# Optimization experiments

Measured on AMD Instinct MI355X. Metric: run time of the kernel, lower is better.

The kernel has to match this reference:

```python
import jax, jax.numpy as jnp
import numpy as np

B, F, S, H = 8, 512, 8192, 8
D = F // H
GROUPS = F // 16  # GroupNorm group_cnt = channels // 16
EPS = 1e-8


def group_norm(x, gamma, beta):
    # x: [B, C, S]; normalize per (group-channels, spatial) like torch GroupNorm
    b, c, s = x.shape
    xg = x.reshape(b, GROUPS, c // GROUPS, s)
    mu = xg.mean(axis=(2, 3), keepdims=True)
    var = xg.var(axis=(2, 3), keepdims=True)
    xn = ((xg - mu) * jax.lax.rsqrt(var + EPS)).reshape(b, c, s)
    return xn * gamma[None, :, None] + beta[None, :, None]


def setup_inputs() -> dict:
    key = jax.random.key(0)
    ks = jax.random.split(key, 5)
    return {
        "hidden_states": jax.random.normal(ks[0], (B, F, S), jnp.float32),
        "qkv_w": jax.random.normal(ks[1], (3, H, D, F), jnp.float32) * 0.02,
        "qkv_b": jnp.zeros((3, 1, 1, H, D), jnp.float32),
        "out_proj": jax.random.normal(ks[2], (F, F), jnp.float32) * 0.02,
        "gn1_gamma": jnp.ones((F,), jnp.float32),
        "gn1_beta": jnp.zeros((F,), jnp.float32),
        "gn2_gamma": jnp.ones((F,), jnp.float32),
        "gn2_beta": jnp.zeros((F,), jnp.float32),
        # torch init is zeros; use small random so the gated branch is exercised
        "gate_g": jax.random.normal(ks[3], (F, 1), jnp.float32) * 0.1,
    }


def reference(hidden_states, qkv_w, qkv_b, out_proj,
              gn1_gamma, gn1_beta, gn2_gamma, gn2_beta, gate_g):
    x = group_norm(hidden_states, gn1_gamma, gn1_beta)
    # [3, B, S, H, D]
    qkv = jnp.einsum('bfl,ihdf->iblhd', x, qkv_w) + qkv_b
    q = jax.nn.elu(qkv[0]) + 1.0
    k = jax.nn.elu(qkv[1]) + 1.0
    v = qkv[2]
    # global non-causal linear attention: KV = sum_l k_l v_l^T  -> [B,H,D,D]
    kv = jnp.einsum('blhf,blhF->bhFf', k, v)
    k_sum = jnp.sum(k, axis=1, keepdims=True)               # [B,1,H,D]
    z = jnp.sum(q * k_sum, axis=-1, keepdims=True)          # [B,S,H,1]
    qz = q / z
    out = jnp.einsum('blhf,bhFf->blhF', qz, kv)             # [B,S,H,D]
    out = out.reshape(out.shape[0], out.shape[1], -1)       # [B,S,F]
    y = jnp.einsum('blf,Ff->bFl', out, out_proj)            # [B,F,S]
    y = group_norm(y, gn2_gamma, gn2_beta)
    # rezero-style gate: residual + per-channel gate * branch
    return hidden_states + gate_g[None] * y
```

## Files before the change

### kernel.cpp

```cpp
#include <hip/hip_runtime.h>
#include <hip/hip_bf16.h>

#define BB 8
#define FF 512
#define SS 8192
#define HH 8
#define DD 64
#define N1 1536

typedef __hip_bfloat16 bf16;
typedef __attribute__((ext_vector_type(8))) short bf16x8;
typedef __attribute__((ext_vector_type(4))) float f32x4;

__device__ __forceinline__ float us2f(unsigned short u) {
    union { unsigned int i; float f; } x; x.i = ((unsigned int)u) << 16; return x.f;
}
__device__ __forceinline__ unsigned short f2b(float f) {
    unsigned int u = __builtin_bit_cast(unsigned int, f);
    return (unsigned short)((u + 0x7FFFu + ((u >> 16) & 1u)) >> 16);
}
__device__ __forceinline__ void gll16(const void* g, void* l) {
    __builtin_amdgcn_global_load_lds((const __attribute__((address_space(1))) void*)g,
                                     (__attribute__((address_space(3))) void*)l, 16, 0, 0);
}
__device__ __forceinline__ bf16x8 fragld(const unsigned short* base, int row, int quad) {
    int off = row * 32 + (((quad + (row >> 1)) & 3) << 3);
    return *(const bf16x8*)(base + off);
}

__global__ void gn1_part(const float* __restrict__ hid, float* __restrict__ part) {
    int bg = blockIdx.x;
    const float4* base = (const float4*)(hid + ((size_t)(bg >> 5) * FF + (bg & 31) * 16) * SS);
    float s = 0.f, s2 = 0.f;
    int t0 = blockIdx.y * 4096 + threadIdx.x;
    #pragma unroll
    for (int it = 0; it < 16; it++) {
        float4 x = base[t0 + it * 256];
        s  += x.x + x.y + x.z + x.w;
        s2 += x.x * x.x + x.y * x.y + x.z * x.z + x.w * x.w;
    }
    #pragma unroll
    for (int off = 32; off > 0; off >>= 1) {
        s  += __shfl_down(s, off, 64);
        s2 += __shfl_down(s2, off, 64);
    }
    __shared__ float rs_[8];
    int wid = threadIdx.x >> 6, lane = threadIdx.x & 63;
    if (lane == 0) { rs_[wid] = s; rs_[wid + 4] = s2; }
    __syncthreads();
    if (threadIdx.x == 0)
        atomicAdd(&part[bg * 2], rs_[0] + rs_[1] + rs_[2] + rs_[3]);
    else if (threadIdx.x == 64)
        atomicAdd(&part[bg * 2 + 1], rs_[4] + rs_[5] + rs_[6] + rs_[7]);
}

__global__ void gn2_part(const unsigned short* __restrict__ y, float* __restrict__ part) {
    int bg = blockIdx.x;
    const bf16x8* base = (const bf16x8*)(y + ((size_t)(bg >> 5) * FF + (bg & 31) * 16) * SS);
    float s = 0.f, s2 = 0.f;
    int t0 = blockIdx.y * 2048 + threadIdx.x;
    #pragma unroll
    for (int it = 0; it < 8; it++) {
        bf16x8 u = base[t0 + it * 256];
        #pragma unroll
        for (int k = 0; k < 8; k++) {
            float a = us2f((unsigned short)u[k]);
            s += a; s2 += a * a;
        }
    }
    #pragma unroll
    for (int off = 32; off > 0; off >>= 1) {
        s  += __shfl_down(s, off, 64);
        s2 += __shfl_down(s2, off, 64);
    }
    __shared__ float rs_[8];
    int wid = threadIdx.x >> 6, lane = threadIdx.x & 63;
    if (lane == 0) { rs_[wid] = s; rs_[wid + 4] = s2; }
    __syncthreads();
    if (threadIdx.x == 0)
        atomicAdd(&part[bg * 2], rs_[0] + rs_[1] + rs_[2] + rs_[3]);
    else if (threadIdx.x == 64)
        atomicAdd(&part[bg * 2 + 1], rs_[4] + rs_[5] + rs_[6] + rs_[7]);
}

__global__ void gn_final(const float* __restrict__ part, const float* __restrict__ gamma,
                         const float* __restrict__ beta, const float* __restrict__ gate,
                         float* __restrict__ sc, float* __restrict__ sh) {
    int c = blockIdx.x * 256 + threadIdx.x;
    int ch = c & 511;
    int bg = (c >> 9) * 32 + (ch >> 4);
    float ts = part[bg * 2], ts2 = part[bg * 2 + 1];
    float mu  = ts * (1.f / 131072.f);
    float var = ts2 * (1.f / 131072.f) - mu * mu;
    float r   = rsqrtf(var + 1e-8f);
    float scv = gamma[ch] * r;
    float shv = beta[ch] - mu * scv;
    if (gate) { float gv = gate[ch]; scv *= gv; shv *= gv; }
    sc[c] = scv; sh[c] = shv;
}

__global__ void castb(const float* __restrict__ s, unsigned short* __restrict__ d, int n4) {
    int i = blockIdx.x * 256 + threadIdx.x;
    if (i >= n4) return;
    float4 v = ((const float4*)s)[i];
    ushort4 u = make_ushort4(f2b(v.x), f2b(v.y), f2b(v.z), f2b(v.w));
    ((ushort4*)d)[i] = u;
}

__global__ void xn_prep(const float* __restrict__ hid, const float* __restrict__ sc,
                        const float* __restrict__ sh, unsigned short* __restrict__ xnA) {
    int b = blockIdx.z, f0 = blockIdx.y * 64, l0 = blockIdx.x * 64;
    __shared__ float t[64][65];
    int tid = threadIdx.x;
    #pragma unroll
    for (int it = 0; it < 16; it++) {
        int idx = it * 256 + tid;
        int f = idx >> 6, l = idx & 63;
        int fg = f0 + f;
        t[f][l] = hid[((size_t)b * FF + fg) * SS + l0 + l] * sc[b * FF + fg] + sh[b * FF + fg];
    }
    __syncthreads();
    #pragma unroll
    for (int it = 0; it < 4; it++) {
        int idx = it * 256 + tid;
        int l = idx >> 4, fq = (idx & 15) * 4;
        ushort4 u = make_ushort4(f2b(t[fq + 0][l]), f2b(t[fq + 1][l]),
                                 f2b(t[fq + 2][l]), f2b(t[fq + 3][l]));
        *(ushort4*)(xnA + ((size_t)b * SS + l0 + l) * FF + f0 + fq) = u;
    }
}

__global__ __launch_bounds__(256) void gemm1_mfma(
    const unsigned short* __restrict__ A, const unsigned short* __restrict__ Bw,
    const float* __restrict__ bias,
    unsigned short* __restrict__ q, unsigned short* __restrict__ kT,
    unsigned short* __restrict__ vT) {
    __shared__ unsigned short smem[16384] __attribute__((aligned(16)));
    unsigned short* As = smem;
    unsigned short* Bs = smem + 4096;
    const int b = blockIdx.z;
    const int m0 = blockIdx.x * 128, n0 = blockIdx.y * 128;
    const int tid = threadIdx.x;
    const int w = tid >> 6, ln = tid & 63;
    const int wr = w >> 1, wc = w & 1;
    const int lrow = ln & 15, quad = ln >> 4;

    const int ch0 = tid, ch1 = tid + 256;
    const int r0 = ch0 >> 2, c0 = ((ch0 & 3) - (r0 >> 1)) & 3;
    const int r1 = ch1 >> 2, c1 = ((ch1 & 3) - (r1 >> 1)) & 3;
    const unsigned short* pA0 = A + ((size_t)b * SS + m0 + r0) * FF + c0 * 8;
    const unsigned short* pA1 = A + ((size_t)b * SS + m0 + r1) * FF + c1 * 8;
    const unsigned short* pB0 = Bw + (size_t)(n0 + r0) * FF + c0 * 8;
    const unsigned short* pB1 = Bw + (size_t)(n0 + r1) * FF + c1 * 8;
    unsigned short* lA0 = As + ch0 * 8; unsigned short* lA1 = As + ch1 * 8;
    unsigned short* lB0 = Bs + ch0 * 8; unsigned short* lB1 = Bs + ch1 * 8;

    f32x4 acc[4][4];
    #pragma unroll
    for (int j = 0; j < 4; j++)
        #pragma unroll
        for (int i = 0; i < 4; i++) acc[j][i] = (f32x4){0.f, 0.f, 0.f, 0.f};

    for (int kk = 0; kk < 16; kk++) {
        gll16(pA0, lA0); gll16(pA1, lA1); gll16(pB0, lB0); gll16(pB1, lB1);
        pA0 += 32; pA1 += 32; pB0 += 32; pB1 += 32;
        __syncthreads();
        bf16x8 af[4], bm[4];
        #pragma unroll
        for (int j = 0; j < 4; j++) af[j] = fragld(Bs, wc * 64 + j * 16 + lrow, quad);
        #pragma unroll
        for (int i = 0; i < 4; i++) bm[i] = fragld(As, wr * 64 + i * 16 + lrow, quad);
        #pragma unroll
        for (int j = 0; j < 4; j++)
            #pragma unroll
            for (int i = 0; i < 4; i++)
                acc[j][i] = __builtin_amdgcn_mfma_f32_16x16x32_bf16(af[j], bm[i], acc[j][i], 0, 0, 0);
        __syncthreads();
    }
    const int n0v = n0 + wc * 64;
    const int sel = n0 >> 9;
    if (sel == 0) {
        const int nchb = (wc << 3) + (quad >> 1);
        const int nin  = (quad & 1) << 2;
        #pragma unroll
        for (int j = 0; j < 4; j++) {
            const float* bp = bias + n0v + j * 16 + (quad << 2);
            float b0 = bp[0], b1 = bp[1], b2 = bp[2], b3 = bp[3];
            #pragma unroll
            for (int i = 0; i < 4; i++) {
                float v0 = acc[j][i][0] + b0, v1 = acc[j][i][1] + b1;
                float v2 = acc[j][i][2] + b2, v3 = acc[j][i][3] + b3;
                v0 = v0 > 0.f ? v0 + 1.f : __expf(v0);
                v1 = v1 > 0.f ? v1 + 1.f : __expf(v1);
                v2 = v2 > 0.f ? v2 + 1.f : __expf(v2);
                v3 = v3 > 0.f ? v3 + 1.f : __expf(v3);
                int m = (wr << 6) + (i << 4) + lrow;
                int chk = (nchb + (j << 1)) ^ (m & 7);
                *(ushort4*)(smem + m * 128 + (chk << 3) + nin) =
                    make_ushort4(f2b(v0), f2b(v1), f2b(v2), f2b(v3));
            }
        }
        __syncthreads();
        const size_t rowb = (size_t)b * SS + m0;
        const int cc = tid & 15, rr = tid >> 4;
        #pragma unroll
        for (int p = 0; p < 8; p++) {
            int m = (p << 4) + rr;
            bf16x8 v = *(const bf16x8*)(smem + m * 128 + ((cc ^ (m & 7)) << 3));
            *(bf16x8*)(q + (rowb + m) * FF + n0 + (cc << 3)) = v;
        }
    } else {
        unsigned short* outp = (sel == 1) ? kT : vT;
        const int nbase = n0 & 511;
        #pragma unroll
        for (int j = 0; j < 4; j++) {
            const float* bp = bias + n0v + j * 16 + (quad << 2);
            float bb[4] = {bp[0], bp[1], bp[2], bp[3]};
            #pragma unroll
            for (int i = 0; i < 4; i++) {
                int m = (wr << 6) + (i << 4) + lrow;
                int mch = m >> 3, mi = m & 7;
                #pragma unroll
                for (int r = 0; r < 4; r++) {
                    float val = acc[j][i][r] + bb[r];
                    if (sel == 1) val = val > 0.f ? val + 1.f : __expf(val);
                    int n = (wc << 6) + (j << 4) + (quad << 2) + r;
                    smem[n * 128 + ((mch ^ ((n >> 2) & 7)) << 3) + mi] = f2b(val);
                }
            }
        }
        __syncthreads();
        const int cc = tid & 15, rr = tid >> 4;
        #pragma unroll
        for (int p = 0; p < 8; p++) {
            int n = (p << 4) + rr;
            bf16x8 v = *(const bf16x8*)(smem + n * 128 + ((cc ^ ((n >> 2) & 7)) << 3));
            int nrel = nbase + n;
            *(bf16x8*)(outp + (((size_t)b * HH + (nrel >> 6)) * DD + (nrel & 63)) * SS
                       + m0 + (cc << 3)) = v;
        }
    }
}

__global__ __launch_bounds__(256) void kv_mfma(
    const unsigned short* __restrict__ kT, const unsigned short* __restrict__ vT,
    float* __restrict__ kv, float* __restrict__ ksum) {
    const int bh = blockIdx.x;
    const int l0 = blockIdx.y * 512;
    const int tid = threadIdx.x;

    {
        int f = tid >> 2, part = tid & 3;
        const unsigned short* kp = kT + ((size_t)bh * DD + f) * SS + l0 + part * 128;
        float s = 0.f;
        #pragma unroll
        for (int c = 0; c < 16; c++) {
            bf16x8 u = *(const bf16x8*)(kp + c * 8);
            #pragma unroll
            for (int j = 0; j < 8; j++) s += us2f((unsigned short)u[j]);
        }
        s += __shfl_down(s, 1, 64);
        s += __shfl_down(s, 2, 64);
        if (part == 0) atomicAdd(&ksum[bh * DD + f], s);
    }

    const int w = tid >> 6, ln = tid & 63;
    const int lrow = ln & 15, quad = ln >> 4;
    f32x4 acc[4];
    #pragma unroll
    for (int ft = 0; ft < 4; ft++) acc[ft] = (f32x4){0.f, 0.f, 0.f, 0.f};
    const unsigned short* vbase = vT + ((size_t)bh * DD + w * 16 + lrow) * SS + l0;
    const unsigned short* kbase = kT + ((size_t)bh * DD + lrow) * SS + l0;
    for (int ks = 0; ks < 16; ks++) {
        bf16x8 vf = *(const bf16x8*)(vbase + ks * 32 + quad * 8);
        #pragma unroll
        for (int ft = 0; ft < 4; ft++) {
            bf16x8 kf = *(const bf16x8*)(kbase + (size_t)(ft * 16) * SS + ks * 32 + quad * 8);
            acc[ft] = __builtin_amdgcn_mfma_f32_16x16x32_bf16(vf, kf, acc[ft], 0, 0, 0);
        }
    }
    float* kvp = kv + (size_t)bh * 4096;
    #pragma unroll
    for (int ft = 0; ft < 4; ft++) {
        #pragma unroll
        for (int r = 0; r < 4; r++) {
            int e = w * 16 + (quad << 2) + r;
            int f = ft * 16 + lrow;
            atomicAdd(&kvp[e * 64 + f], acc[ft][r]);
        }
    }
}

__global__ void kvcast(const float* __restrict__ kv, unsigned short* __restrict__ kv16) {
    int i = blockIdx.x * 256 + threadIdx.x;
    float4 v = ((const float4*)kv)[i];
    ((ushort4*)kv16)[i] = make_ushort4(f2b(v.x), f2b(v.y), f2b(v.z), f2b(v.w));
}

__global__ __launch_bounds__(256) void attn_mfma(
    const unsigned short* __restrict__ q, const unsigned short* __restrict__ kv16,
    const float* __restrict__ ksum, unsigned short* __restrict__ attn) {
    const int bh = blockIdx.y, b = bh >> 3, h = bh & 7;
    const int l0 = blockIdx.x * 128;
    __shared__ float ksS[64];
    __shared__ float zS[128];
    const int tid = threadIdx.x;
    if (tid < 64) ksS[tid] = ksum[bh * DD + tid];
    __syncthreads();
    if (tid < 128) {
        const unsigned short* qp = q + ((size_t)b * SS + l0 + tid) * FF + h * DD;
        float z = 0.f;
        #pragma unroll
        for (int c = 0; c < 8; c++) {
            bf16x8 u = *(const bf16x8*)(qp + c * 8);
            #pragma unroll
            for (int j = 0; j < 8; j++) z += us2f((unsigned short)u[j]) * ksS[c * 8 + j];
        }
        zS[tid] = 1.f / z;
    }
    __syncthreads();

    const int w = tid >> 6, ln = tid & 63;
    const int lrow = ln & 15, quad = ln >> 4;
    const unsigned short* kvp = kv16 + (size_t)bh * 4096;
    bf16x8 kvf[4][2];
    #pragma unroll
    for (int et = 0; et < 4; et++)
        #pragma unroll
        for (int ks = 0; ks < 2; ks++)
            kvf[et][ks] = *(const bf16x8*)(kvp + (et * 16 + lrow) * 64 + ks * 32 + quad * 8);

    f32x4 acc[2][4];
    #pragma unroll
    for (int lt = 0; lt < 2; lt++)
        #pragma unroll
        for (int et = 0; et < 4; et++) acc[lt][et] = (f32x4){0.f, 0.f, 0.f, 0.f};

    const unsigned short* qbase = q + ((size_t)b * SS + l0 + w * 32) * FF + h * DD;
    #pragma unroll
    for (int lt = 0; lt < 2; lt++) {
        #pragma unroll
        for (int ks = 0; ks < 2; ks++) {
            bf16x8 qf = *(const bf16x8*)(qbase + (size_t)(lt * 16 + lrow) * FF + ks * 32 + quad * 8);
            #pragma unroll
            for (int et = 0; et < 4; et++)
                acc[lt][et] = __builtin_amdgcn_mfma_f32_16x16x32_bf16(kvf[et][ks], qf, acc[lt][et], 0, 0, 0);
        }
    }
    #pragma unroll
    for (int lt = 0; lt < 2; lt++) {
        int lloc = w * 32 + lt * 16 + lrow;
        float zi = zS[lloc];
        unsigned short* op = attn + ((size_t)b * SS + l0 + lloc) * FF + h * DD;
        #pragma unroll
        for (int et = 0; et < 4; et++) {
            ushort4 u = make_ushort4(f2b(acc[lt][et][0] * zi), f2b(acc[lt][et][1] * zi),
                                     f2b(acc[lt][et][2] * zi), f2b(acc[lt][et][3] * zi));
            *(ushort4*)(op + et * 16 + (quad << 2)) = u;
        }
    }
}

__global__ __launch_bounds__(256) void gemm2_mfma(
    const unsigned short* __restrict__ A, const unsigned short* __restrict__ Bw,
    unsigned short* __restrict__ y) {
    __shared__ unsigned short smem[16384] __attribute__((aligned(16)));
    unsigned short* As = smem;
    unsigned short* Bs = smem + 4096;
    const int b = blockIdx.z;
    const int m0 = blockIdx.x * 128, n0 = blockIdx.y * 128;
    const int tid = threadIdx.x;
    const int w = tid >> 6, ln = tid & 63;
    const int wr = w >> 1, wc = w & 1;
    const int lrow = ln & 15, quad = ln >> 4;

    const int ch0 = tid, ch1 = tid + 256;
    const int r0 = ch0 >> 2, c0 = ((ch0 & 3) - (r0 >> 1)) & 3;
    const int r1 = ch1 >> 2, c1 = ((ch1 & 3) - (r1 >> 1)) & 3;
    const unsigned short* pA0 = A + ((size_t)b * SS + m0 + r0) * FF + c0 * 8;
    const unsigned short* pA1 = A + ((size_t)b * SS + m0 + r1) * FF + c1 * 8;
    const unsigned short* pB0 = Bw + (size_t)(n0 + r0) * FF + c0 * 8;
    const unsigned short* pB1 = Bw + (size_t)(n0 + r1) * FF + c1 * 8;
    unsigned short* lA0 = As + ch0 * 8; unsigned short* lA1 = As + ch1 * 8;
    unsigned short* lB0 = Bs + ch0 * 8; unsigned short* lB1 = Bs + ch1 * 8;

    f32x4 acc[4][4];
    #pragma unroll
    for (int i = 0; i < 4; i++)
        #pragma unroll
        for (int j = 0; j < 4; j++) acc[i][j] = (f32x4){0.f, 0.f, 0.f, 0.f};

    for (int kk = 0; kk < 16; kk++) {
        gll16(pA0, lA0); gll16(pA1, lA1); gll16(pB0, lB0); gll16(pB1, lB1);
        pA0 += 32; pA1 += 32; pB0 += 32; pB1 += 32;
        __syncthreads();
        bf16x8 am[4], bn[4];
        #pragma unroll
        for (int i = 0; i < 4; i++) am[i] = fragld(As, wr * 64 + i * 16 + lrow, quad);
        #pragma unroll
        for (int j = 0; j < 4; j++) bn[j] = fragld(Bs, wc * 64 + j * 16 + lrow, quad);
        #pragma unroll
        for (int i = 0; i < 4; i++)
            #pragma unroll
            for (int j = 0; j < 4; j++)
                acc[i][j] = __builtin_amdgcn_mfma_f32_16x16x32_bf16(am[i], bn[j], acc[i][j], 0, 0, 0);
        __syncthreads();
    }
    #pragma unroll
    for (int i = 0; i < 4; i++) {
        const int mch = (wr << 3) + (i << 1) + (quad >> 1);
        const int min_ = (quad & 1) << 2;
        #pragma unroll
        for (int j = 0; j < 4; j++) {
            int n = (wc << 6) + (j << 4) + lrow;
            int chk = mch ^ (n & 7);
            *(ushort4*)(smem + n * 128 + (chk << 3) + min_) =
                make_ushort4(f2b(acc[i][j][0]), f2b(acc[i][j][1]),
                             f2b(acc[i][j][2]), f2b(acc[i][j][3]));
        }
    }
    __syncthreads();
    const int cc = tid & 15, rr = tid >> 4;
    #pragma unroll
    for (int p = 0; p < 8; p++) {
        int n = (p << 4) + rr;
        bf16x8 v = *(const bf16x8*)(smem + n * 128 + ((cc ^ (n & 7)) << 3));
        *(bf16x8*)(y + ((size_t)b * FF + n0 + n) * SS + m0 + (cc << 3)) = v;
    }
}

__global__ void final_kernel(const float* __restrict__ hid, const bf16* __restrict__ y,
                             const float* __restrict__ gsc, const float* __restrict__ gsh,
                             float* __restrict__ out) {
    int bf = blockIdx.x;
    float a = gsc[bf], c0 = gsh[bf];
    const float4*  hp = (const float4*)(hid + (size_t)bf * SS);
    const ushort4* yp = (const ushort4*)(y + (size_t)bf * SS);
    float4* op = (float4*)(out + (size_t)bf * SS);
    for (int t = threadIdx.x; t < 2048; t += 256) {
        float4 hv = hp[t];
        ushort4 yv = yp[t];
        float4 r;
        r.x = hv.x + a * us2f(yv.x) + c0;
        r.y = hv.y + a * us2f(yv.y) + c0;
        r.z = hv.z + a * us2f(yv.z) + c0;
        r.w = hv.w + a * us2f(yv.w) + c0;
        op[t] = r;
    }
}

extern "C" void kernel_launch(void* const* d_in, const int* in_sizes, int n_in,
                              void* d_out, int out_size, void* d_ws, size_t ws_size,
                              hipStream_t stream) {
    const float* hid      = (const float*)d_in[0];
    const float* qkv_w    = (const float*)d_in[1];
    const float* qkv_b    = (const float*)d_in[2];
    const float* out_proj = (const float*)d_in[3];
    const float* g1       = (const float*)d_in[4];
    const float* b1       = (const float*)d_in[5];
    const float* g2       = (const float*)d_in[6];
    const float* b2       = (const float*)d_in[7];
    const float* gate     = (const float*)d_in[8];
    float* out = (float*)d_out;

    char* p = (char*)d_ws;
    float* sc1 = (float*)p; p += (size_t)4096 * 4;
    float* sh1 = (float*)p; p += (size_t)4096 * 4;
    float* gsc = (float*)p; p += (size_t)4096 * 4;
    float* gsh = (float*)p; p += (size_t)4096 * 4;
    float* kvb = (float*)p; p += (size_t)262144 * 4;
    float* ksm = (float*)p; p += (size_t)4096 * 4;
    float* gnp = (float*)p; p += (size_t)1024 * 4;
    unsigned short* kv16 = (unsigned short*)p; p += (size_t)262144 * 2;
    unsigned short* Wb = (unsigned short*)p; p += (size_t)786432 * 2;
    unsigned short* Pb = (unsigned short*)p; p += (size_t)262144 * 2;
    unsigned short* qb = (unsigned short*)p; p += (size_t)33554432 * 2;
    unsigned short* kTb = (unsigned short*)p; p += (size_t)33554432 * 2;
    unsigned short* vTb = (unsigned short*)p;
    unsigned short* attn = kTb;
    unsigned short* yb   = vTb;
    unsigned short* xnA  = (unsigned short*)d_out;

    hipMemsetAsync(kvb, 0, (size_t)(262144 + 4096 + 1024) * 4, stream);

    gn1_part<<<dim3(256, 8), 256, 0, stream>>>(hid, gnp);
    gn_final<<<16, 256, 0, stream>>>(gnp, g1, b1, nullptr, sc1, sh1);
    castb<<<768, 256, 0, stream>>>(qkv_w, Wb, 196608);
    castb<<<256, 256, 0, stream>>>(out_proj, Pb, 65536);
    xn_prep<<<dim3(128, 8, 8), 256, 0, stream>>>(hid, sc1, sh1, xnA);
    gemm1_mfma<<<dim3(64, 12, 8), 256, 0, stream>>>(xnA, Wb, qkv_b, qb, kTb, vTb);
    kv_mfma<<<dim3(64, 16), 256, 0, stream>>>(kTb, vTb, kvb, ksm);
    kvcast<<<256, 256, 0, stream>>>(kvb, kv16);
    attn_mfma<<<dim3(64, 64), 256, 0, stream>>>(qb, kv16, ksm, attn);
    gemm2_mfma<<<dim3(64, 4, 8), 256, 0, stream>>>(attn, Pb, yb);
    gn2_part<<<dim3(256, 8), 256, 0, stream>>>((const unsigned short*)yb, gnp + 512);
    gn_final<<<16, 256, 0, stream>>>(gnp + 512, g2, b2, gate, gsc, gsh);
    final_kernel<<<4096, 256, 0, stream>>>(hid, (const bf16*)yb, gsc, gsh, out);
}
```

Before: 651.6 us.

## Fuse GroupNorm2 stats into gemm2 epilogue, widen K tiles, split gemm1 by output

The GroupNorm2 partial-sum reduction now runs in the gemm2 epilogue, using shuffle reductions and atomics, so the separate gn2_part pass over y is removed. Both GEMMs now load 64-wide K tiles with an XOR swizzle, which halves the number of loop iterations and barriers. gemm1 is split into two template instantiations. The K/V instance swaps the MFMA operand order so its accumulators can be written straight to the transposed kT/vT layout. Both GEMM epilogues drop the LDS staging and write ushort4 directly to global memory, which may give less coalesced stores. The fused epilogue also adds more atomics.

```diff
diff --git a/kernel.cpp b/kernel.cpp
--- a/kernel.cpp
+++ b/kernel.cpp
@@ -23,9 +23,8 @@
     __builtin_amdgcn_global_load_lds((const __attribute__((address_space(1))) void*)g,
                                      (__attribute__((address_space(3))) void*)l, 16, 0, 0);
 }
-__device__ __forceinline__ bf16x8 fragld(const unsigned short* base, int row, int quad) {
-    int off = row * 32 + (((quad + (row >> 1)) & 3) << 3);
-    return *(const bf16x8*)(base + off);
+__device__ __forceinline__ bf16x8 fragld64(const unsigned short* base, int row, int kq) {
+    return *(const bf16x8*)(base + row * 64 + ((kq ^ (row & 7)) << 3));
 }
 
 __global__ void gn1_part(const float* __restrict__ hid, float* __restrict__ part) {
@@ -38,35 +37,6 @@
         float4 x = base[t0 + it * 256];
         s  += x.x + x.y + x.z + x.w;
         s2 += x.x * x.x + x.y * x.y + x.z * x.z + x.w * x.w;
-    }
-    #pragma unroll
-    for (int off = 32; off > 0; off >>= 1) {
-        s  += __shfl_down(s, off, 64);
-        s2 += __shfl_down(s2, off, 64);
-    }
-    __shared__ float rs_[8];
-    int wid = threadIdx.x >> 6, lane = threadIdx.x & 63;
-    if (lane == 0) { rs_[wid] = s; rs_[wid + 4] = s2; }
-    __syncthreads();
-    if (threadIdx.x == 0)
-        atomicAdd(&part[bg * 2], rs_[0] + rs_[1] + rs_[2] + rs_[3]);
-    else if (threadIdx.x == 64)
-        atomicAdd(&part[bg * 2 + 1], rs_[4] + rs_[5] + rs_[6] + rs_[7]);
-}
-
-__global__ void gn2_part(const unsigned short* __restrict__ y, float* __restrict__ part) {
-    int bg = blockIdx.x;
-    const bf16x8* base = (const bf16x8*)(y + ((size_t)(bg >> 5) * FF + (bg & 31) * 16) * SS);
-    float s = 0.f, s2 = 0.f;
-    int t0 = blockIdx.y * 2048 + threadIdx.x;
-    #pragma unroll
-    for (int it = 0; it < 8; it++) {
-        bf16x8 u = base[t0 + it * 256];
-        #pragma unroll
-        for (int k = 0; k < 8; k++) {
-            float a = us2f((unsigned short)u[k]);
-            s += a; s2 += a * a;
-        }
     }
     #pragma unroll
     for (int off = 32; off > 0; off >>= 1) {
@@ -130,30 +100,32 @@
     }
 }
 
+template<int KV>
 __global__ __launch_bounds__(256) void gemm1_mfma(
     const unsigned short* __restrict__ A, const unsigned short* __restrict__ Bw,
     const float* __restrict__ bias,
     unsigned short* __restrict__ q, unsigned short* __restrict__ kT,
     unsigned short* __restrict__ vT) {
-    __shared__ unsigned short smem[16384] __attribute__((aligned(16)));
-    unsigned short* As = smem;
-    unsigned short* Bs = smem + 4096;
+    __shared__ unsigned short As[8192] __attribute__((aligned(16)));
+    __shared__ unsigned short Bs[8192] __attribute__((aligned(16)));
     const int b = blockIdx.z;
-    const int m0 = blockIdx.x * 128, n0 = blockIdx.y * 128;
+    const int m0 = blockIdx.x * 128;
+    const int n0 = (KV ? 512 : 0) + blockIdx.y * 128;
     const int tid = threadIdx.x;
     const int w = tid >> 6, ln = tid & 63;
     const int wr = w >> 1, wc = w & 1;
     const int lrow = ln & 15, quad = ln >> 4;
 
-    const int ch0 = tid, ch1 = tid + 256;
-    const int r0 = ch0 >> 2, c0 = ((ch0 & 3) - (r0 >> 1)) & 3;
-    const int r1 = ch1 >> 2, c1 = ((ch1 & 3) - (r1 >> 1)) & 3;
-    const unsigned short* pA0 = A + ((size_t)b * SS + m0 + r0) * FF + c0 * 8;
-    const unsigned short* pA1 = A + ((size_t)b * SS + m0 + r1) * FF + c1 * 8;
-    const unsigned short* pB0 = Bw + (size_t)(n0 + r0) * FF + c0 * 8;
-    const unsigned short* pB1 = Bw + (size_t)(n0 + r1) * FF + c1 * 8;
-    unsigned short* lA0 = As + ch0 * 8; unsigned short* lA1 = As + ch1 * 8;
-    unsigned short* lB0 = Bs + ch0 * 8; unsigned short* lB1 = Bs + ch1 * 8;
+    const unsigned short* pA[4];
+    const unsigned short* pB[4];
+    #pragma unroll
+    for (int u = 0; u < 4; u++) {
+        int ch = tid + u * 256;
+        int r = ch >> 3;
+        int cg = (ch & 7) ^ (r & 7);
+        pA[u] = A + ((size_t)b * SS + m0 + r) * FF + cg * 8;
+        pB[u] = Bw + (size_t)(n0 + r) * FF + cg * 8;
+    }
 
     f32x4 acc[4][4];
     #pragma unroll
@@ -161,27 +133,41 @@
         #pragma unroll
         for (int i = 0; i < 4; i++) acc[j][i] = (f32x4){0.f, 0.f, 0.f, 0.f};
 
-    for (int kk = 0; kk < 16; kk++) {
-        gll16(pA0, lA0); gll16(pA1, lA1); gll16(pB0, lB0); gll16(pB1, lB1);
-        pA0 += 32; pA1 += 32; pB0 += 32; pB1 += 32;
+    for (int kk = 0; kk < 8; kk++) {
+        #pragma unroll
+        for (int u = 0; u < 4; u++) {
+            gll16(pA[u], As + (tid + u * 256) * 8);
+            gll16(pB[u], Bs + (tid + u * 256) * 8);
+            pA[u] += 64; pB[u] += 64;
+        }
         __syncthreads();
-        bf16x8 af[4], bm[4];
-        #pragma unroll
-        for (int j = 0; j < 4; j++) af[j] = fragld(Bs, wc * 64 + j * 16 + lrow, quad);
-        #pragma unroll
-        for (int i = 0; i < 4; i++) bm[i] = fragld(As, wr * 64 + i * 16 + lrow, quad);
-        #pragma unroll
-        for (int j = 0; j < 4; j++)
-            #pragma unroll
-            for (int i = 0; i < 4; i++)
-                acc[j][i] = __builtin_amdgcn_mfma_f32_16x16x32_bf16(af[j], bm[i], acc[j][i], 0, 0, 0);
+        #pragma unroll
+        for (int s = 0; s < 2; s++) {
+            bf16x8 af[4], bm[4];
+            #pragma unroll
+            for (int j = 0; j < 4; j++) af[j] = fragld64(Bs, wc * 64 + j * 16 + lrow, s * 4 + quad);
+            #pragma unroll
+            for (int i = 0; i < 4; i++) bm[i] = fragld64(As, wr * 64 + i * 16 + lrow, s * 4 + quad);
+            if constexpr (KV == 0) {
+                #pragma unroll
+                for (int j = 0; j < 4; j++)
+                    #pragma unroll
+                    for (int i = 0; i < 4; i++)
+                        acc[j][i] = __builtin_amdgcn_mfma_f32_16x16x32_bf16(af[j], bm[i], acc[j][i], 0, 0, 0);
+            } else {
+                #pragma unroll
+                for (int i = 0; i < 4; i++)
+                    #pragma unroll
+                    for (int j = 0; j < 4; j++)
+                        acc[i][j] = __builtin_amdgcn_mfma_f32_16x16x32_bf16(bm[i], af[j], acc[i][j], 0, 0, 0);
+            }
+        }
         __syncthreads();
     }
-    const int n0v = n0 + wc * 64;
-    const int sel = n0 >> 9;
-    if (sel == 0) {
-        const int nchb = (wc << 3) + (quad >> 1);
-        const int nin  = (quad & 1) << 2;
+
+    if constexpr (KV == 0) {
+        const int n0v = n0 + wc * 64;
+        const size_t mrow = (size_t)b * SS + m0 + wr * 64 + lrow;
         #pragma unroll
         for (int j = 0; j < 4; j++) {
             const float* bp = bias + n0v + j * 16 + (quad << 2);
@@ -194,50 +180,33 @@
                 v1 = v1 > 0.f ? v1 + 1.f : __expf(v1);
                 v2 = v2 > 0.f ? v2 + 1.f : __expf(v2);
                 v3 = v3 > 0.f ? v3 + 1.f : __expf(v3);
-                int m = (wr << 6) + (i << 4) + lrow;
-                int chk = (nchb + (j << 1)) ^ (m & 7);
-                *(ushort4*)(smem + m * 128 + (chk << 3) + nin) =
+                *(ushort4*)(q + (mrow + i * 16) * FF + n0v + j * 16 + (quad << 2)) =
                     make_ushort4(f2b(v0), f2b(v1), f2b(v2), f2b(v3));
             }
         }
-        __syncthreads();
-        const size_t rowb = (size_t)b * SS + m0;
-        const int cc = tid & 15, rr = tid >> 4;
-        #pragma unroll
-        for (int p = 0; p < 8; p++) {
-            int m = (p << 4) + rr;
-            bf16x8 v = *(const bf16x8*)(smem + m * 128 + ((cc ^ (m & 7)) << 3));
-            *(bf16x8*)(q + (rowb + m) * FF + n0 + (cc << 3)) = v;
-        }
     } else {
-        unsigned short* outp = (sel == 1) ? kT : vT;
-        const int nbase = n0 & 511;
+        const bool isk = (n0 < 1024);
+        unsigned short* outp = isk ? kT : vT;
+        const int m_base = m0 + wr * 64 + (quad << 2);
         #pragma unroll
         for (int j = 0; j < 4; j++) {
-            const float* bp = bias + n0v + j * 16 + (quad << 2);
-            float bb[4] = {bp[0], bp[1], bp[2], bp[3]};
+            const int nabs = n0 + (wc << 6) + (j << 4) + lrow;
+            const int nq = nabs & 511;
+            const float bv = bias[nabs];
+            unsigned short* orow = outp + (((size_t)b * HH + (nq >> 6)) * DD + (nq & 63)) * SS;
             #pragma unroll
             for (int i = 0; i < 4; i++) {
-                int m = (wr << 6) + (i << 4) + lrow;
-                int mch = m >> 3, mi = m & 7;
-                #pragma unroll
-                for (int r = 0; r < 4; r++) {
-                    float val = acc[j][i][r] + bb[r];
-                    if (sel == 1) val = val > 0.f ? val + 1.f : __expf(val);
-                    int n = (wc << 6) + (j << 4) + (quad << 2) + r;
-                    smem[n * 128 + ((mch ^ ((n >> 2) & 7)) << 3) + mi] = f2b(val);
+                float v0 = acc[i][j][0] + bv, v1 = acc[i][j][1] + bv;
+                float v2 = acc[i][j][2] + bv, v3 = acc[i][j][3] + bv;
+                if (isk) {
+                    v0 = v0 > 0.f ? v0 + 1.f : __expf(v0);
+                    v1 = v1 > 0.f ? v1 + 1.f : __expf(v1);
+                    v2 = v2 > 0.f ? v2 + 1.f : __expf(v2);
+                    v3 = v3 > 0.f ? v3 + 1.f : __expf(v3);
                 }
+                *(ushort4*)(orow + m_base + i * 16) =
+                    make_ushort4(f2b(v0), f2b(v1), f2b(v2), f2b(v3));
             }
-        }
-        __syncthreads();
-        const int cc = tid & 15, rr = tid >> 4;
-        #pragma unroll
-        for (int p = 0; p < 8; p++) {
-            int n = (p << 4) + rr;
-            bf16x8 v = *(const bf16x8*)(smem + n * 128 + ((cc ^ ((n >> 2) & 7)) << 3));
-            int nrel = nbase + n;
-            *(bf16x8*)(outp + (((size_t)b * HH + (nrel >> 6)) * DD + (nrel & 63)) * SS
-                       + m0 + (cc << 3)) = v;
         }
     }
 }
@@ -363,10 +332,9 @@
 
 __global__ __launch_bounds__(256) void gemm2_mfma(
     const unsigned short* __restrict__ A, const unsigned short* __restrict__ Bw,
-    unsigned short* __restrict__ y) {
-    __shared__ unsigned short smem[16384] __attribute__((aligned(16)));
-    unsigned short* As = smem;
-    unsigned short* Bs = smem + 4096;
+    unsigned short* __restrict__ y, float* __restrict__ gpart) {
+    __shared__ unsigned short As[8192] __attribute__((aligned(16)));
+    __shared__ unsigned short Bs[8192] __attribute__((aligned(16)));
     const int b = blockIdx.z;
     const int m0 = blockIdx.x * 128, n0 = blockIdx.y * 128;
     const int tid = threadIdx.x;
@@ -374,15 +342,16 @@
     const int wr = w >> 1, wc = w & 1;
     const int lrow = ln & 15, quad = ln >> 4;
 
-    const int ch0 = tid, ch1 = tid + 256;
-    const int r0 = ch0 >> 2, c0 = ((ch0 & 3) - (r0 >> 1)) & 3;
-    const int r1 = ch1 >> 2, c1 = ((ch1 & 3) - (r1 >> 1)) & 3;
-    const unsigned short* pA0 = A + ((size_t)b * SS + m0 + r0) * FF + c0 * 8;
-    const unsigned short* pA1 = A + ((size_t)b * SS + m0 + r1) * FF + c1 * 8;
-    const unsigned short* pB0 = Bw + (size_t)(n0 + r0) * FF + c0 * 8;
-    const unsigned short* pB1 = Bw + (size_t)(n0 + r1) * FF + c1 * 8;
-    unsigned short* lA0 = As + ch0 * 8; unsigned short* lA1 = As + ch1 * 8;
-    unsigned short* lB0 = Bs + ch0 * 8; unsigned short* lB1 = Bs + ch1 * 8;
+    const unsigned short* pA[4];
+    const unsigned short* pB[4];
+    #pragma unroll
+    for (int u = 0; u < 4; u++) {
+        int ch = tid + u * 256;
+        int r = ch >> 3;
+        int cg = (ch & 7) ^ (r & 7);
+        pA[u] = A + ((size_t)b * SS + m0 + r) * FF + cg * 8;
+        pB[u] = Bw + (size_t)(n0 + r) * FF + cg * 8;
+    }
 
     f32x4 acc[4][4];
     #pragma unroll
@@ -390,42 +359,52 @@
         #pragma unroll
         for (int j = 0; j < 4; j++) acc[i][j] = (f32x4){0.f, 0.f, 0.f, 0.f};
 
-    for (int kk = 0; kk < 16; kk++) {
-        gll16(pA0, lA0); gll16(pA1, lA1); gll16(pB0, lB0); gll16(pB1, lB1);
-        pA0 += 32; pA1 += 32; pB0 += 32; pB1 += 32;
+    for (int kk = 0; kk < 8; kk++) {
+        #pragma unroll
+        for (int u = 0; u < 4; u++) {
+            gll16(pA[u], As + (tid + u * 256) * 8);
+            gll16(pB[u], Bs + (tid + u * 256) * 8);
+            pA[u] += 64; pB[u] += 64;
+        }
         __syncthreads();
-        bf16x8 am[4], bn[4];
-        #pragma unroll
-        for (int i = 0; i < 4; i++) am[i] = fragld(As, wr * 64 + i * 16 + lrow, quad);
-        #pragma unroll
-        for (int j = 0; j < 4; j++) bn[j] = fragld(Bs, wc * 64 + j * 16 + lrow, quad);
-        #pragma unroll
-        for (int i = 0; i < 4; i++)
-            #pragma unroll
-            for (int j = 0; j < 4; j++)
-                acc[i][j] = __builtin_amdgcn_mfma_f32_16x16x32_bf16(am[i], bn[j], acc[i][j], 0, 0, 0);
+        #pragma unroll
+        for (int s = 0; s < 2; s++) {
+            bf16x8 am[4], bn[4];
+            #pragma unroll
+            for (int i = 0; i < 4; i++) am[i] = fragld64(As, wr * 64 + i * 16 + lrow, s * 4 + quad);
+            #pragma unroll
+            for (int j = 0; j < 4; j++) bn[j] = fragld64(Bs, wc * 64 + j * 16 + lrow, s * 4 + quad);
+            #pragma unroll
+            for (int i = 0; i < 4; i++)
+                #pragma unroll
+                for (int j = 0; j < 4; j++)
+                    acc[i][j] = __builtin_amdgcn_mfma_f32_16x16x32_bf16(am[i], bn[j], acc[i][j], 0, 0, 0);
+        }
         __syncthreads();
     }
-    #pragma unroll
-    for (int i = 0; i < 4; i++) {
-        const int mch = (wr << 3) + (i << 1) + (quad >> 1);
-        const int min_ = (quad & 1) << 2;
-        #pragma unroll
-        for (int j = 0; j < 4; j++) {
-            int n = (wc << 6) + (j << 4) + lrow;
-            int chk = mch ^ (n & 7);
-            *(ushort4*)(smem + n * 128 + (chk << 3) + min_) =
-                make_ushort4(f2b(acc[i][j][0]), f2b(acc[i][j][1]),
-                             f2b(acc[i][j][2]), f2b(acc[i][j][3]));
-        }
-    }
-    __syncthreads();
-    const int cc = tid & 15, rr = tid >> 4;
-    #pragma unroll
-    for (int p = 0; p < 8; p++) {
-        int n = (p << 4) + rr;
-        bf16x8 v = *(const bf16x8*)(smem + n * 128 + ((cc ^ (n & 7)) << 3));
-        *(bf16x8*)(y + ((size_t)b * FF + n0 + n) * SS + m0 + (cc << 3)) = v;
+    const int m_base = m0 + (wr << 6) + (quad << 2);
+    #pragma unroll
+    for (int j = 0; j < 4; j++) {
+        const int n = n0 + (wc << 6) + (j << 4) + lrow;
+        unsigned short* orow = y + ((size_t)b * FF + n) * SS + m_base;
+        float sj = 0.f, s2j = 0.f;
+        #pragma unroll
+        for (int i = 0; i < 4; i++) {
+            float v0 = acc[i][j][0], v1 = acc[i][j][1], v2 = acc[i][j][2], v3 = acc[i][j][3];
+            sj  += v0 + v1 + v2 + v3;
+            s2j += v0 * v0 + v1 * v1 + v2 * v2 + v3 * v3;
+            *(ushort4*)(orow + i * 16) = make_ushort4(f2b(v0), f2b(v1), f2b(v2), f2b(v3));
+        }
+        #pragma unroll
+        for (int off = 32; off > 0; off >>= 1) {
+            sj  += __shfl_down(sj, off, 64);
+            s2j += __shfl_down(s2j, off, 64);
+        }
+        if (ln == 0) {
+            int g = (n0 + (wc << 6) + (j << 4)) >> 4;
+            atomicAdd(&gpart[(b * 32 + g) * 2],     sj);
+            atomicAdd(&gpart[(b * 32 + g) * 2 + 1], s2j);
+        }
     }
 }
 
@@ -488,12 +467,12 @@
     castb<<<768, 256, 0, stream>>>(qkv_w, Wb, 196608);
     castb<<<256, 256, 0, stream>>>(out_proj, Pb, 65536);
     xn_prep<<<dim3(128, 8, 8), 256, 0, stream>>>(hid, sc1, sh1, xnA);
-    gemm1_mfma<<<dim3(64, 12, 8), 256, 0, stream>>>(xnA, Wb, qkv_b, qb, kTb, vTb);
+    gemm1_mfma<0><<<dim3(64, 4, 8), 256, 0, stream>>>(xnA, Wb, qkv_b, qb, kTb, vTb);
+    gemm1_mfma<1><<<dim3(64, 8, 8), 256, 0, stream>>>(xnA, Wb, qkv_b, qb, kTb, vTb);
     kv_mfma<<<dim3(64, 16), 256, 0, stream>>>(kTb, vTb, kvb, ksm);
     kvcast<<<256, 256, 0, stream>>>(kvb, kv16);
     attn_mfma<<<dim3(64, 64), 256, 0, stream>>>(qb, kv16, ksm, attn);
-    gemm2_mfma<<<dim3(64, 4, 8), 256, 0, stream>>>(attn, Pb, yb);
-    gn2_part<<<dim3(256, 8), 256, 0, stream>>>((const unsigned short*)yb, gnp + 512);
+    gemm2_mfma<<<dim3(64, 4, 8), 256, 0, stream>>>(attn, Pb, yb, gnp + 512);
     gn_final<<<16, 256, 0, stream>>>(gnp + 512, g2, b2, gate, gsc, gsh);
     final_kernel<<<4096, 256, 0, stream>>>(hid, (const bf16*)yb, gsc, gsh, out);
 }
```

Result: slower. 741.6 us (+13.8%).
